# Optimization experiments

Measured on AMD Instinct MI355X. Metric: run time of the kernel, lower is better.

Reference implementation:

```python
import jax, jax.numpy as jnp
import numpy as np

N_EDGES = 262144
N_TRIP = 1048576
D = 128
N_RBF = 6
A_DIM = 49  # n_spher * l_spher
N_BIL = 8


def setup_inputs() -> dict:
    key = jax.random.key(0)
    ks = jax.random.split(key, 16)
    s = lambda fan_in: 1.0 / np.sqrt(fan_in)
    return {
        "m_ji": jax.random.normal(ks[0], (N_EDGES, D), jnp.float32),
        "e_rbf": jax.random.normal(ks[1], (N_EDGES, N_RBF), jnp.float32),
        "a_sbf": jax.random.normal(ks[2], (N_TRIP, A_DIM), jnp.float32),
        "nbr_list": jax.random.randint(ks[3], (N_EDGES, 2), 0, 100000),
        "angle_list": jax.random.randint(ks[4], (N_TRIP, 3), 0, N_EDGES),
        "kj_idx": jax.random.randint(ks[5], (N_TRIP,), 0, N_EDGES),
        "nbr_m_w": jax.random.normal(ks[6], (D, D), jnp.float32) * s(D),
        "nbr_m_b": jnp.zeros((D,), jnp.float32),
        "e_rbf_w": jax.random.normal(ks[7], (N_RBF, D), jnp.float32) * s(N_RBF),
        "a_sbf_w": jax.random.normal(ks[8], (A_DIM, N_BIL), jnp.float32) * s(A_DIM),
        "final_w": jax.random.normal(ks[9], (D, N_BIL, D), jnp.float32) * s(N_BIL * D),
        "m_ji_w": jax.random.normal(ks[10], (D, D), jnp.float32) * s(D),
        "m_ji_b": jnp.zeros((D,), jnp.float32),
        "post_w": jax.random.normal(ks[11], (D, D), jnp.float32) * s(D),
        "post_b": jnp.zeros((D,), jnp.float32),
        "res_w": jax.random.normal(ks[12], (3, 2, D, D), jnp.float32) * s(D),
        "res_b": jnp.zeros((3, 2, D), jnp.float32),
    }


def _residual(x, w2, b2):
    # two Dense(swish) layers + skip
    out = x
    for k in range(2):
        out = jax.nn.silu(out @ w2[k] + b2[k])
    return out + x


def reference(m_ji, e_rbf, a_sbf, nbr_list, angle_list, kj_idx,
              nbr_m_w, nbr_m_b, e_rbf_w, a_sbf_w, final_w,
              m_ji_w, m_ji_b, post_w, post_b, res_w, res_b):
    # DirectedMessage: gather per-triplet edge features
    t_m = jax.nn.silu(m_ji[kj_idx] @ nbr_m_w + nbr_m_b)   # [W, D]
    t_e = e_rbf[kj_idx] @ e_rbf_w                          # [W, D]
    m_and_e = t_m * t_e                                    # [W, D]
    t_a = a_sbf @ a_sbf_w                                  # [W, J]
    out = jnp.einsum('wj,wl,ijl->wi', t_a, m_and_e, final_w)  # [W, D]
    directed = jax.ops.segment_sum(out, kj_idx, num_segments=m_ji.shape[0])  # [E, D]

    transf_m_ji = jax.nn.silu(m_ji @ m_ji_w + m_ji_b)
    output = directed + transf_m_ji
    output = _residual(output, res_w[0], res_b[0])
    output = jax.nn.silu(output @ post_w + post_b) + transf_m_ji
    output = _residual(output, res_w[1], res_b[1])
    output = _residual(output, res_w[2], res_b[2])
    return output
```

## Files before the change

kernel.cpp:

```cpp
#include <hip/hip_runtime.h>

#define N_EDGE 262144
#define N_TRI  1048576
#define DIM    128
#define NRBF   6
#define ADIM   49
#define NBIL   8
#define TE     64
#define TP     2
#define NTHR   256
#define SXD    68
#define EB2    2048
#define NSL    4

typedef __attribute__((ext_vector_type(8))) short bf16x8;
typedef __attribute__((ext_vector_type(4))) float f32x4;

__device__ __forceinline__ float fast_rcp(float x) {
    float r; asm("v_rcp_f32 %0, %1" : "=v"(r) : "v"(x)); return r;
}
__device__ __forceinline__ float fast_exp2(float x) {
    float r; asm("v_exp_f32 %0, %1" : "=v"(r) : "v"(x)); return r;
}
__device__ __forceinline__ float silu_f(float x) {
    return x * fast_rcp(1.f + fast_exp2(-1.44269504f * x));
}
__device__ __forceinline__ unsigned short f2bf(float f) {
    unsigned int u = __float_as_uint(f);
    return (unsigned short)((u + 0x7FFFu + ((u >> 16) & 1u)) >> 16);
}
__device__ __forceinline__ unsigned int pk2(float x, float y) {
    unsigned int r;
    asm("v_cvt_pk_bf16_f32 %0, %1, %2" : "=v"(r) : "v"(x), "v"(y));
    return r;
}
__device__ __forceinline__ float bf2f(unsigned short u) {
    return __uint_as_float(((unsigned int)u) << 16);
}

__global__ __launch_bounds__(256) void prep_w_k(
    const float* __restrict__ nbr, const float* __restrict__ mji,
    const float* __restrict__ post, const float* __restrict__ res,
    const float* __restrict__ fw, unsigned short* __restrict__ wt)
{
    int idx = blockIdx.x * 256 + threadIdx.x;
    if (idx < 9 * 16384) {
        int m = idx >> 14, rr = idx & 16383;
        int n = rr >> 7, ks = rr & 127;
        int ko = (ks & ~31) | ((ks & 1) << 4) | ((ks >> 1) & 15);
        const float* src = (m == 0) ? nbr : (m == 1) ? mji : (m == 2) ? post
                          : (res + (size_t)(m - 3) * 16384);
        wt[idx] = f2bf(src[ko * DIM + n]);
    } else {
        int r2 = idx - 9 * 16384;
        int n = r2 >> 10, j = (r2 >> 7) & 7, ls = r2 & 127;
        int lo = (ls & ~31) | ((ls & 1) << 4) | ((ls >> 1) & 15);
        wt[idx] = f2bf(fw[(size_t)(n * NBIL + j) * DIM + lo]);
    }
}

__global__ __launch_bounds__(256) void ta_all_k(
    const float* __restrict__ a_sbf, const float* __restrict__ a_sbf_w,
    float* __restrict__ taw)
{
    __shared__ __align__(16) float sA[256 * ADIM];
    __shared__ float sWa[ADIM * NBIL];
    const int tid = threadIdx.x;
    const size_t w0 = (size_t)blockIdx.x * 256;

    {
        const float4* src = (const float4*)(a_sbf + w0 * ADIM);
        float4* dst = (float4*)sA;
        for (int i = tid; i < (256 * ADIM) / 4; i += 256) dst[i] = src[i];
    }
    for (int i = tid; i < ADIM * NBIL; i += 256) sWa[i] = a_sbf_w[i];
    __syncthreads();

    float ta[NBIL];
    #pragma unroll
    for (int j = 0; j < NBIL; ++j) ta[j] = 0.0f;
    const float* row = sA + tid * ADIM;
    #pragma unroll
    for (int k = 0; k < ADIM; ++k) {
        float v = row[k];
        #pragma unroll
        for (int j = 0; j < NBIL; ++j) ta[j] = fmaf(v, sWa[k * NBIL + j], ta[j]);
    }
    float4* dst = (float4*)(taw + (w0 + tid) * NBIL);
    dst[0] = make_float4(ta[0], ta[1], ta[2], ta[3]);
    dst[1] = make_float4(ta[4], ta[5], ta[6], ta[7]);
}

__global__ __launch_bounds__(1024) void seg_reduce_k(
    const float* __restrict__ taw, const int* __restrict__ kj_idx,
    float* __restrict__ ta_sum)
{
    __shared__ float acc[EB2 * NBIL];
    const int tid = threadIdx.x;
    const int eg = blockIdx.x >> 2;
    const int sl = blockIdx.x & 3;
    const int lo = eg * EB2;

    for (int i = tid; i < EB2 * NBIL; i += 1024) acc[i] = 0.f;
    __syncthreads();

    const int4* kj4 = (const int4*)kj_idx;
    const int i0 = sl * (N_TRI / 4 / NSL);
    const int i1 = i0 + (N_TRI / 4 / NSL);
    for (int i = i0 + tid; i < i1; i += 1024) {
        int4 v = kj4[i];
        int w0 = i * 4;
        #pragma unroll
        for (int k = 0; k < 4; ++k) {
            int e = (k == 0) ? v.x : (k == 1) ? v.y : (k == 2) ? v.z : v.w;
            unsigned d = (unsigned)(e - lo);
            if (d < (unsigned)EB2) {
                const float4* p = (const float4*)(taw + (size_t)(w0 + k) * NBIL);
                float4 a = p[0], b = p[1];
                float* q = acc + d * NBIL;
                atomicAdd(q + 0, a.x); atomicAdd(q + 1, a.y);
                atomicAdd(q + 2, a.z); atomicAdd(q + 3, a.w);
                atomicAdd(q + 4, b.x); atomicAdd(q + 5, b.y);
                atomicAdd(q + 6, b.z); atomicAdd(q + 7, b.w);
            }
        }
    }
    __syncthreads();
    for (int i = tid; i < EB2 * NBIL; i += 1024)
        unsafeAtomicAdd(ta_sum + (size_t)lo * NBIL + i, acc[i]);
}

__global__ __launch_bounds__(256) void triplet_atomic_k(
    const float* __restrict__ a_sbf, const float* __restrict__ a_sbf_w,
    const int* __restrict__ kj_idx, float* __restrict__ ta_sum)
{
    __shared__ __align__(16) float sA[256 * ADIM];
    __shared__ float sWa[ADIM * NBIL];
    const int tid = threadIdx.x;
    const size_t w0 = (size_t)blockIdx.x * 256;
    {
        const float4* src = (const float4*)(a_sbf + w0 * ADIM);
        float4* dst = (float4*)sA;
        for (int i = tid; i < (256 * ADIM) / 4; i += 256) dst[i] = src[i];
    }
    for (int i = tid; i < ADIM * NBIL; i += 256) sWa[i] = a_sbf_w[i];
    __syncthreads();
    float ta[NBIL];
    #pragma unroll
    for (int j = 0; j < NBIL; ++j) ta[j] = 0.0f;
    const float* row = sA + tid * ADIM;
    #pragma unroll
    for (int k = 0; k < ADIM; ++k) {
        float v = row[k];
        #pragma unroll
        for (int j = 0; j < NBIL; ++j) ta[j] = fmaf(v, sWa[k * NBIL + j], ta[j]);
    }
    const int e = kj_idx[w0 + tid];
    float* dst = ta_sum + (size_t)e * NBIL;
    #pragma unroll
    for (int j = 0; j < NBIL; ++j) unsafeAtomicAdd(dst + j, ta[j]);
}

__global__ __launch_bounds__(NTHR) void edge_main_k(
    const float* __restrict__ m_ji, const float* __restrict__ e_rbf,
    const float* __restrict__ ta_sum, const unsigned short* __restrict__ wt,
    const float* __restrict__ nbr_m_b, const float* __restrict__ e_rbf_w,
    const float* __restrict__ m_ji_b, const float* __restrict__ post_b,
    const float* __restrict__ res_b, float* __restrict__ out)
{
    __shared__ __align__(16) unsigned int sXdA[TP * TE * SXD];
    __shared__ __align__(16) unsigned int sTdA[TP * TE * SXD];
    __shared__ __align__(16) float sTAT[NBIL * TP * TE];
    __shared__ __align__(16) float sET[NRBF * TP * TE];

    const int tid  = threadIdx.x;
    const int lane = tid & 63;
    const int ml   = lane & 15;
    const int g    = lane >> 4;
    const int wq   = tid >> 6;
    const int n0   = wq * 32;
    const int q16  = wq * 16;
    const size_t e0 = (size_t)blockIdx.x * (TP * TE);
    const int ET = TP * TE;

    bf16x8 A[4][2], Bf[2][4];
    f32x4 acc0[4][2], acc1[4][2], xr0[4][2], xr1[4][2], bs0, bs1;

    auto prefB = [&](const unsigned short* wtm, int ldk, int kbase) {
        #pragma unroll
        for (int nt = 0; nt < 2; ++nt) {
            const unsigned short* wb =
                wtm + (size_t)(n0 + nt * 16 + ml) * ldk + kbase + g * 8;
            #pragma unroll
            for (int ks = 0; ks < 4; ++ks)
                Bf[nt][ks] = *(const bf16x8*)(wb + ks * 32);
        }
    };
    auto ldbias = [&](const float* bp) {
        float b0 = bp[n0 + ml], b1 = bp[n0 + 16 + ml];
        bs0[0] = b0; bs0[1] = b0; bs0[2] = b0; bs0[3] = b0;
        bs1[0] = b1; bs1[1] = b1; bs1[2] = b1; bs1[3] = b1;
    };
    auto ldzero = [&]() {
        #pragma unroll
        for (int r = 0; r < 4; ++r) { bs0[r] = 0.f; bs1[r] = 0.f; }
    };

    prefB(wt + 1 * 16384, DIM, 0);

    #pragma unroll
    for (int i = 0; i < 8; ++i) {
        int q = tid + i * NTHR;
        int row = q >> 4, sub = q & 15;
        int dq = sub >> 2, c4 = (sub & 3) * 4;
        const float* src = m_ji + (e0 + row) * DIM + dq * 32 + c4;
        float4 a = *(const float4*)(src);
        float4 b = *(const float4*)(src + 16);
        uint4 d;
        d.x = pk2(a.x, b.x); d.y = pk2(a.y, b.y);
        d.z = pk2(a.z, b.z); d.w = pk2(a.w, b.w);
        *(uint4*)(sXdA + row * SXD + dq * 16 + c4) = d;
    }
    #pragma unroll
    for (int i = 0; i < 4; ++i) {
        int idx = tid + i * NTHR;
        int j = idx >> 7, e = idx & 127;
        sTAT[j * ET + e] = ta_sum[(e0 + e) * NBIL + j];
    }
    for (int i = tid; i < NRBF * ET; i += NTHR) {
        int j = i >> 7, e = i & 127;
        sET[j * ET + e] = e_rbf[(e0 + e) * NRBF + j];
    }
    __syncthreads();

    auto loadA = [&](const unsigned int* bufp, int h) {
        const unsigned short* base = (const unsigned short*)bufp;
        #pragma unroll
        for (int mt = 0; mt < 4; ++mt) {
            const unsigned short* rb = base + (mt * 16 + ml) * (SXD * 2) + h * 64 + g * 8;
            A[mt][0] = *(const bf16x8*)(rb);
            A[mt][1] = *(const bf16x8*)(rb + 32);
        }
    };
    auto mfmaH = [&](f32x4 (&acc)[4][2], int h, bool seed) {
        #pragma unroll
        for (int kk = 0; kk < 2; ++kk)
        #pragma unroll
        for (int nt = 0; nt < 2; ++nt)
        #pragma unroll
        for (int mt = 0; mt < 4; ++mt) {
            f32x4 cin = (seed && kk == 0) ? (nt == 0 ? bs0 : bs1) : acc[mt][nt];
            acc[mt][nt] = __builtin_amdgcn_mfma_f32_16x16x32_bf16(
                A[mt][kk], Bf[nt][h * 2 + kk], cin, 0, 0, 0);
        }
    };
    auto gemm_full = [&](const unsigned int* bufp, f32x4 (&acc)[4][2]) {
        loadA(bufp, 0); mfmaH(acc, 0, true); loadA(bufp, 1); mfmaH(acc, 1, false);
    };
    auto store_pair = [&](f32x4 (&v0)[4][2], f32x4 (&v1)[4][2]) {
        __syncthreads();
        #pragma unroll
        for (int mt = 0; mt < 4; ++mt)
        #pragma unroll
        for (int r = 0; r < 4; ++r) {
            int off = (mt * 16 + g * 4 + r) * SXD + q16 + ml;
            sXdA[off]               = pk2(v0[mt][0][r], v0[mt][1][r]);
            sXdA[TE * SXD + off]    = pk2(v1[mt][0][r], v1[mt][1][r]);
        }
        __syncthreads();
    };

    const unsigned int* b0p = sXdA;
    const unsigned int* b1p = sXdA + TE * SXD;

    ldbias(m_ji_b);
    gemm_full(b0p, acc0);
    gemm_full(b1p, acc1);
    prefB(wt + 0 * 16384, DIM, 0);
    #pragma unroll
    for (int mt = 0; mt < 4; ++mt)
    #pragma unroll
    for (int r = 0; r < 4; ++r) {
        int off = (mt * 16 + g * 4 + r) * SXD + q16 + ml;
        sTdA[off]            = pk2(silu_f(acc0[mt][0][r]), silu_f(acc0[mt][1][r]));
        sTdA[TE * SXD + off] = pk2(silu_f(acc1[mt][0][r]), silu_f(acc1[mt][1][r]));
    }

    ldbias(nbr_m_b);
    float ewc[2][NRBF];
    #pragma unroll
    for (int nt = 0; nt < 2; ++nt)
    #pragma unroll
    for (int q = 0; q < NRBF; ++q)
        ewc[nt][q] = e_rbf_w[q * DIM + n0 + nt * 16 + ml];
    gemm_full(b0p, acc0);
    gemm_full(b1p, acc1);
    const unsigned short* fwb = wt + 9 * 16384;
    prefB(fwb, NBIL * DIM, 0);
    #pragma unroll
    for (int t = 0; t < 2; ++t) {
        f32x4 (&ac)[4][2] = (t == 0) ? acc0 : acc1;
        #pragma unroll
        for (int mt = 0; mt < 4; ++mt) {
            f32x4 er[NRBF];
            #pragma unroll
            for (int q = 0; q < NRBF; ++q)
                er[q] = *(const f32x4*)(sET + q * ET + t * TE + mt * 16 + g * 4);
            #pragma unroll
            for (int r = 0; r < 4; ++r) {
                float te0 = 0.f, te1 = 0.f;
                #pragma unroll
                for (int q = 0; q < NRBF; ++q) {
                    te0 = fmaf(er[q][r], ewc[0][q], te0);
                    te1 = fmaf(er[q][r], ewc[1][q], te1);
                }
                ac[mt][0][r] = silu_f(ac[mt][0][r]) * te0;
                ac[mt][1][r] = silu_f(ac[mt][1][r]) * te1;
            }
        }
    }
    store_pair(acc0, acc1);

    #pragma unroll
    for (int mt = 0; mt < 4; ++mt)
    #pragma unroll
    for (int r = 0; r < 4; ++r) {
        int off = (mt * 16 + g * 4 + r) * SXD + q16 + ml;
        unsigned int t0 = sTdA[off], t1 = sTdA[TE * SXD + off];
        xr0[mt][0][r] = bf2f((unsigned short)(t0 & 0xffff));
        xr0[mt][1][r] = bf2f((unsigned short)(t0 >> 16));
        xr1[mt][0][r] = bf2f((unsigned short)(t1 & 0xffff));
        xr1[mt][1][r] = bf2f((unsigned short)(t1 >> 16));
    }
    ldzero();
    for (int j = 0; j < NBIL; ++j) {
        gemm_full(b0p, acc0);
        gemm_full(b1p, acc1);
        if (j < NBIL - 1) prefB(fwb, NBIL * DIM, (j + 1) * DIM);
        else              prefB(wt + 3 * 16384, DIM, 0);
        #pragma unroll
        for (int mt = 0; mt < 4; ++mt) {
            f32x4 tv0 = *(const f32x4*)(sTAT + j * ET + mt * 16 + g * 4);
            f32x4 tv1 = *(const f32x4*)(sTAT + j * ET + TE + mt * 16 + g * 4);
            #pragma unroll
            for (int nt = 0; nt < 2; ++nt)
            #pragma unroll
            for (int r = 0; r < 4; ++r) {
                xr0[mt][nt][r] = fmaf(tv0[r], acc0[mt][nt][r], xr0[mt][nt][r]);
                xr1[mt][nt][r] = fmaf(tv1[r], acc1[mt][nt][r], xr1[mt][nt][r]);
            }
        }
    }
    store_pair(xr0, xr1);

    auto silu_inplace = [&](f32x4 (&ac)[4][2]) {
        #pragma unroll
        for (int mt = 0; mt < 4; ++mt)
        #pragma unroll
        for (int r = 0; r < 4; ++r) {
            ac[mt][0][r] = silu_f(ac[mt][0][r]);
            ac[mt][1][r] = silu_f(ac[mt][1][r]);
        }
    };
    auto add_into = [&](f32x4 (&xr)[4][2], f32x4 (&ac)[4][2]) {
        #pragma unroll
        for (int mt = 0; mt < 4; ++mt)
        #pragma unroll
        for (int r = 0; r < 4; ++r) {
            xr[mt][0][r] += silu_f(ac[mt][0][r]);
            xr[mt][1][r] += silu_f(ac[mt][1][r]);
        }
    };

    ldbias(res_b + 0);
    gemm_full(b0p, acc0); gemm_full(b1p, acc1); prefB(wt + 4 * 16384, DIM, 0);
    silu_inplace(acc0); silu_inplace(acc1);
    store_pair(acc0, acc1);
    ldbias(res_b + 128);
    gemm_full(b0p, acc0); gemm_full(b1p, acc1); prefB(wt + 2 * 16384, DIM, 0);
    add_into(xr0, acc0); add_into(xr1, acc1);
    store_pair(xr0, xr1);

    ldbias(post_b);
    gemm_full(b0p, acc0); gemm_full(b1p, acc1); prefB(wt + 5 * 16384, DIM, 0);
    #pragma unroll
    for (int mt = 0; mt < 4; ++mt)
    #pragma unroll
    for (int r = 0; r < 4; ++r) {
        int off = (mt * 16 + g * 4 + r) * SXD + q16 + ml;
        unsigned int t0 = sTdA[off], t1 = sTdA[TE * SXD + off];
        xr0[mt][0][r] = silu_f(acc0[mt][0][r]) + bf2f((unsigned short)(t0 & 0xffff));
        xr0[mt][1][r] = silu_f(acc0[mt][1][r]) + bf2f((unsigned short)(t0 >> 16));
        xr1[mt][0][r] = silu_f(acc1[mt][0][r]) + bf2f((unsigned short)(t1 & 0xffff));
        xr1[mt][1][r] = silu_f(acc1[mt][1][r]) + bf2f((unsigned short)(t1 >> 16));
    }
    store_pair(xr0, xr1);

    ldbias(res_b + 256);
    gemm_full(b0p, acc0); gemm_full(b1p, acc1); prefB(wt + 6 * 16384, DIM, 0);
    silu_inplace(acc0); silu_inplace(acc1);
    store_pair(acc0, acc1);
    ldbias(res_b + 384);
    gemm_full(b0p, acc0); gemm_full(b1p, acc1); prefB(wt + 7 * 16384, DIM, 0);
    add_into(xr0, acc0); add_into(xr1, acc1);
    store_pair(xr0, xr1);

    ldbias(res_b + 512);
    gemm_full(b0p, acc0); gemm_full(b1p, acc1); prefB(wt + 8 * 16384, DIM, 0);
    silu_inplace(acc0); silu_inplace(acc1);
    store_pair(acc0, acc1);
    ldbias(res_b + 640);
    gemm_full(b0p, acc0); gemm_full(b1p, acc1);
    #pragma unroll
    for (int mt = 0; mt < 4; ++mt)
    #pragma unroll
    for (int r = 0; r < 4; ++r) {
        int row = mt * 16 + g * 4 + r;
        out[(e0 + row) * DIM + n0 + ml]           = silu_f(acc0[mt][0][r]) + xr0[mt][0][r];
        out[(e0 + row) * DIM + n0 + 16 + ml]      = silu_f(acc0[mt][1][r]) + xr0[mt][1][r];
        out[(e0 + TE + row) * DIM + n0 + ml]      = silu_f(acc1[mt][0][r]) + xr1[mt][0][r];
        out[(e0 + TE + row) * DIM + n0 + 16 + ml] = silu_f(acc1[mt][1][r]) + xr1[mt][1][r];
    }
}

extern "C" void kernel_launch(void* const* d_in, const int* in_sizes, int n_in,
                              void* d_out, int out_size, void* d_ws, size_t ws_size,
                              hipStream_t stream)
{
    (void)in_sizes; (void)n_in; (void)out_size;
    const float* m_ji    = (const float*)d_in[0];
    const float* e_rbf   = (const float*)d_in[1];
    const float* a_sbf   = (const float*)d_in[2];
    const int*   kj_idx  = (const int*)d_in[5];
    const float* nbr_m_w = (const float*)d_in[6];
    const float* nbr_m_b = (const float*)d_in[7];
    const float* e_rbf_w = (const float*)d_in[8];
    const float* a_sbf_w = (const float*)d_in[9];
    const float* final_w = (const float*)d_in[10];
    const float* m_ji_w  = (const float*)d_in[11];
    const float* m_ji_b  = (const float*)d_in[12];
    const float* post_w  = (const float*)d_in[13];
    const float* post_b  = (const float*)d_in[14];
    const float* res_w   = (const float*)d_in[15];
    const float* res_b   = (const float*)d_in[16];
    float* out = (float*)d_out;

    const size_t taB  = (size_t)N_EDGE * NBIL * sizeof(float);
    const size_t wtB  = (size_t)278528 * sizeof(unsigned short);
    const size_t tawB = (size_t)N_TRI * NBIL * sizeof(float);

    float* ta_sum = (float*)d_ws;
    unsigned short* wt = (unsigned short*)((char*)d_ws + taB);
    float* taw = (float*)((char*)d_ws + taB + wtB);

    prep_w_k<<<1088, 256, 0, stream>>>(nbr_m_w, m_ji_w, post_w, res_w, final_w, wt);
    hipMemsetAsync(ta_sum, 0, taB, stream);

    if (ws_size >= taB + wtB + tawB) {
        ta_all_k<<<N_TRI / 256, 256, 0, stream>>>(a_sbf, a_sbf_w, taw);
        seg_reduce_k<<<(N_EDGE / EB2) * NSL, 1024, 0, stream>>>(taw, kj_idx, ta_sum);
    } else {
        triplet_atomic_k<<<N_TRI / 256, 256, 0, stream>>>(a_sbf, a_sbf_w, kj_idx, ta_sum);
    }
    edge_main_k<<<N_EDGE / (TP * TE), NTHR, 0, stream>>>(m_ji, e_rbf, ta_sum, wt,
        nbr_m_b, e_rbf_w, m_ji_b, post_b, res_b, out);
}
```

Baseline: 489.0 us.

## Keep residuals in shared bf16 ping-pong buffers to cut register pressure

The fp32 residual accumulators xr0/xr1 no longer live in registers across the post-MLP chain. The residual is kept as bf16 in shared memory and updated in place through two alternating buffers, which also removes one barrier per layer. The transformed m_ji is packed into registers instead of a dedicated shared array. The bilinear loop now runs per 64-row tile, so the final_w fragments are reloaded twice. The intent is lower VGPR use and fewer syncs, at the cost of extra weight loads and residuals rounded to bf16 between layers.

```diff
diff --git a/kernel.cpp b/kernel.cpp
--- a/kernel.cpp
+++ b/kernel.cpp
@@ -8,6 +8,7 @@
 #define NBIL   8
 #define TE     64
 #define TP     2
+#define ET     (TP * TE)
 #define NTHR   256
 #define SXD    68
 #define EB2    2048
@@ -168,10 +169,10 @@
     const float* __restrict__ m_ji_b, const float* __restrict__ post_b,
     const float* __restrict__ res_b, float* __restrict__ out)
 {
-    __shared__ __align__(16) unsigned int sXdA[TP * TE * SXD];
-    __shared__ __align__(16) unsigned int sTdA[TP * TE * SXD];
-    __shared__ __align__(16) float sTAT[NBIL * TP * TE];
-    __shared__ __align__(16) float sET[NRBF * TP * TE];
+    __shared__ __align__(16) unsigned int b0[ET * SXD];
+    __shared__ __align__(16) unsigned int b1[ET * SXD];
+    __shared__ __align__(16) float sTAT[NBIL * ET];
+    __shared__ __align__(16) float sET[NRBF * ET];
 
     const int tid  = threadIdx.x;
     const int lane = tid & 63;
@@ -180,11 +181,11 @@
     const int wq   = tid >> 6;
     const int n0   = wq * 32;
     const int q16  = wq * 16;
-    const size_t e0 = (size_t)blockIdx.x * (TP * TE);
-    const int ET = TP * TE;
+    const size_t e0 = (size_t)blockIdx.x * ET;
 
     bf16x8 A[4][2], Bf[2][4];
-    f32x4 acc0[4][2], acc1[4][2], xr0[4][2], xr1[4][2], bs0, bs1;
+    f32x4 acc0[4][2], acc1[4][2], bs0, bs1;
+    unsigned int trp0[4][4], trp1[4][4];
 
     auto prefB = [&](const unsigned short* wtm, int ldk, int kbase) {
         #pragma unroll
@@ -197,9 +198,9 @@
         }
     };
     auto ldbias = [&](const float* bp) {
-        float b0 = bp[n0 + ml], b1 = bp[n0 + 16 + ml];
-        bs0[0] = b0; bs0[1] = b0; bs0[2] = b0; bs0[3] = b0;
-        bs1[0] = b1; bs1[1] = b1; bs1[2] = b1; bs1[3] = b1;
+        float v0 = bp[n0 + ml], v1 = bp[n0 + 16 + ml];
+        bs0[0] = v0; bs0[1] = v0; bs0[2] = v0; bs0[3] = v0;
+        bs1[0] = v1; bs1[1] = v1; bs1[2] = v1; bs1[3] = v1;
     };
     auto ldzero = [&]() {
         #pragma unroll
@@ -219,7 +220,7 @@
         uint4 d;
         d.x = pk2(a.x, b.x); d.y = pk2(a.y, b.y);
         d.z = pk2(a.z, b.z); d.w = pk2(a.w, b.w);
-        *(uint4*)(sXdA + row * SXD + dq * 16 + c4) = d;
+        *(uint4*)(b0 + row * SXD + dq * 16 + c4) = d;
     }
     #pragma unroll
     for (int i = 0; i < 4; ++i) {
@@ -233,11 +234,12 @@
     }
     __syncthreads();
 
-    auto loadA = [&](const unsigned int* bufp, int h) {
+    auto loadA = [&](const unsigned int* bufp, int t, int h) {
         const unsigned short* base = (const unsigned short*)bufp;
         #pragma unroll
         for (int mt = 0; mt < 4; ++mt) {
-            const unsigned short* rb = base + (mt * 16 + ml) * (SXD * 2) + h * 64 + g * 8;
+            const unsigned short* rb =
+                base + (t * 64 + mt * 16 + ml) * (SXD * 2) + h * 64 + g * 8;
             A[mt][0] = *(const bf16x8*)(rb);
             A[mt][1] = *(const bf16x8*)(rb + 32);
         }
@@ -254,172 +256,194 @@
                 A[mt][kk], Bf[nt][h * 2 + kk], cin, 0, 0, 0);
         }
     };
-    auto gemm_full = [&](const unsigned int* bufp, f32x4 (&acc)[4][2]) {
-        loadA(bufp, 0); mfmaH(acc, 0, true); loadA(bufp, 1); mfmaH(acc, 1, false);
-    };
-    auto store_pair = [&](f32x4 (&v0)[4][2], f32x4 (&v1)[4][2]) {
-        __syncthreads();
+    auto gemm_full = [&](const unsigned int* bufp, int t, f32x4 (&acc)[4][2]) {
+        loadA(bufp, t, 0); mfmaH(acc, 0, true);
+        loadA(bufp, t, 1); mfmaH(acc, 1, false);
+    };
+    auto store_tile = [&](unsigned int* bufp, int t, f32x4 (&v)[4][2]) {
         #pragma unroll
         for (int mt = 0; mt < 4; ++mt)
         #pragma unroll
-        for (int r = 0; r < 4; ++r) {
-            int off = (mt * 16 + g * 4 + r) * SXD + q16 + ml;
-            sXdA[off]               = pk2(v0[mt][0][r], v0[mt][1][r]);
-            sXdA[TE * SXD + off]    = pk2(v1[mt][0][r], v1[mt][1][r]);
-        }
-        __syncthreads();
-    };
-
-    const unsigned int* b0p = sXdA;
-    const unsigned int* b1p = sXdA + TE * SXD;
+        for (int r = 0; r < 4; ++r)
+            bufp[(t * 64 + mt * 16 + g * 4 + r) * SXD + q16 + ml] =
+                pk2(v[mt][0][r], v[mt][1][r]);
+    };
 
     ldbias(m_ji_b);
-    gemm_full(b0p, acc0);
-    gemm_full(b1p, acc1);
+    gemm_full(b0, 0, acc0);
+    gemm_full(b0, 1, acc1);
     prefB(wt + 0 * 16384, DIM, 0);
     #pragma unroll
     for (int mt = 0; mt < 4; ++mt)
     #pragma unroll
     for (int r = 0; r < 4; ++r) {
-        int off = (mt * 16 + g * 4 + r) * SXD + q16 + ml;
-        sTdA[off]            = pk2(silu_f(acc0[mt][0][r]), silu_f(acc0[mt][1][r]));
-        sTdA[TE * SXD + off] = pk2(silu_f(acc1[mt][0][r]), silu_f(acc1[mt][1][r]));
+        trp0[mt][r] = pk2(silu_f(acc0[mt][0][r]), silu_f(acc0[mt][1][r]));
+        trp1[mt][r] = pk2(silu_f(acc1[mt][0][r]), silu_f(acc1[mt][1][r]));
     }
 
     ldbias(nbr_m_b);
-    float ewc[2][NRBF];
-    #pragma unroll
-    for (int nt = 0; nt < 2; ++nt)
-    #pragma unroll
-    for (int q = 0; q < NRBF; ++q)
-        ewc[nt][q] = e_rbf_w[q * DIM + n0 + nt * 16 + ml];
-    gemm_full(b0p, acc0);
-    gemm_full(b1p, acc1);
+    gemm_full(b0, 0, acc0);
+    gemm_full(b0, 1, acc1);
     const unsigned short* fwb = wt + 9 * 16384;
     prefB(fwb, NBIL * DIM, 0);
+    {
+        float ewc[2][NRBF];
+        #pragma unroll
+        for (int nt = 0; nt < 2; ++nt)
+        #pragma unroll
+        for (int q = 0; q < NRBF; ++q)
+            ewc[nt][q] = e_rbf_w[q * DIM + n0 + nt * 16 + ml];
+        #pragma unroll
+        for (int t = 0; t < 2; ++t) {
+            f32x4 (&ac)[4][2] = (t == 0) ? acc0 : acc1;
+            #pragma unroll
+            for (int mt = 0; mt < 4; ++mt) {
+                f32x4 er[NRBF];
+                #pragma unroll
+                for (int q = 0; q < NRBF; ++q)
+                    er[q] = *(const f32x4*)(sET + q * ET + t * 64 + mt * 16 + g * 4);
+                #pragma unroll
+                for (int r = 0; r < 4; ++r) {
+                    float te0 = 0.f, te1 = 0.f;
+                    #pragma unroll
+                    for (int q = 0; q < NRBF; ++q) {
+                        te0 = fmaf(er[q][r], ewc[0][q], te0);
+                        te1 = fmaf(er[q][r], ewc[1][q], te1);
+                    }
+                    ac[mt][0][r] = silu_f(ac[mt][0][r]) * te0;
+                    ac[mt][1][r] = silu_f(ac[mt][1][r]) * te1;
+                }
+            }
+        }
+    }
+    store_tile(b1, 0, acc0);
+    store_tile(b1, 1, acc1);
+    __syncthreads();
+
+    ldzero();
     #pragma unroll
     for (int t = 0; t < 2; ++t) {
+        f32x4 xr[4][2];
+        #pragma unroll
+        for (int mt = 0; mt < 4; ++mt)
+        #pragma unroll
+        for (int r = 0; r < 4; ++r) {
+            unsigned int tv = (t == 0) ? trp0[mt][r] : trp1[mt][r];
+            xr[mt][0][r] = bf2f((unsigned short)(tv & 0xffff));
+            xr[mt][1][r] = bf2f((unsigned short)(tv >> 16));
+        }
+        for (int j = 0; j < NBIL; ++j) {
+            gemm_full(b1, t, acc0);
+            if (j < NBIL - 1)      prefB(fwb, NBIL * DIM, (j + 1) * DIM);
+            else if (t == 0)       prefB(fwb, NBIL * DIM, 0);
+            else                   prefB(wt + 3 * 16384, DIM, 0);
+            #pragma unroll
+            for (int mt = 0; mt < 4; ++mt) {
+                f32x4 tv = *(const f32x4*)(sTAT + j * ET + t * 64 + mt * 16 + g * 4);
+                #pragma unroll
+                for (int nt = 0; nt < 2; ++nt)
+                #pragma unroll
+                for (int r = 0; r < 4; ++r)
+                    xr[mt][nt][r] = fmaf(tv[r], acc0[mt][nt][r], xr[mt][nt][r]);
+            }
+        }
+        store_tile(b0, t, xr);
+    }
+    __syncthreads();
+
+    auto silu_both = [&]() {
+        #pragma unroll
+        for (int mt = 0; mt < 4; ++mt)
+        #pragma unroll
+        for (int r = 0; r < 4; ++r) {
+            acc0[mt][0][r] = silu_f(acc0[mt][0][r]);
+            acc0[mt][1][r] = silu_f(acc0[mt][1][r]);
+            acc1[mt][0][r] = silu_f(acc1[mt][0][r]);
+            acc1[mt][1][r] = silu_f(acc1[mt][1][r]);
+        }
+    };
+    auto xupdate = [&](unsigned int* xbuf) {
+        #pragma unroll
+        for (int t = 0; t < 2; ++t)
+        #pragma unroll
+        for (int mt = 0; mt < 4; ++mt)
+        #pragma unroll
+        for (int r = 0; r < 4; ++r) {
+            int off = (t * 64 + mt * 16 + g * 4 + r) * SXD + q16 + ml;
+            unsigned int xo = xbuf[off];
+            f32x4 (&ac)[4][2] = (t == 0) ? acc0 : acc1;
+            float v0 = bf2f((unsigned short)(xo & 0xffff)) + silu_f(ac[mt][0][r]);
+            float v1 = bf2f((unsigned short)(xo >> 16))    + silu_f(ac[mt][1][r]);
+            xbuf[off] = pk2(v0, v1);
+        }
+        __syncthreads();
+    };
+
+    ldbias(res_b + 0);
+    gemm_full(b0, 0, acc0); gemm_full(b0, 1, acc1);
+    prefB(wt + 4 * 16384, DIM, 0);
+    silu_both();
+    store_tile(b1, 0, acc0); store_tile(b1, 1, acc1);
+    __syncthreads();
+
+    ldbias(res_b + 128);
+    gemm_full(b1, 0, acc0); gemm_full(b1, 1, acc1);
+    prefB(wt + 2 * 16384, DIM, 0);
+    xupdate(b0);
+
+    ldbias(post_b);
+    gemm_full(b0, 0, acc0); gemm_full(b0, 1, acc1);
+    prefB(wt + 5 * 16384, DIM, 0);
+    #pragma unroll
+    for (int t = 0; t < 2; ++t)
+    #pragma unroll
+    for (int mt = 0; mt < 4; ++mt)
+    #pragma unroll
+    for (int r = 0; r < 4; ++r) {
+        int off = (t * 64 + mt * 16 + g * 4 + r) * SXD + q16 + ml;
+        unsigned int tv = (t == 0) ? trp0[mt][r] : trp1[mt][r];
         f32x4 (&ac)[4][2] = (t == 0) ? acc0 : acc1;
-        #pragma unroll
-        for (int mt = 0; mt < 4; ++mt) {
-            f32x4 er[NRBF];
-            #pragma unroll
-            for (int q = 0; q < NRBF; ++q)
-                er[q] = *(const f32x4*)(sET + q * ET + t * TE + mt * 16 + g * 4);
-            #pragma unroll
-            for (int r = 0; r < 4; ++r) {
-                float te0 = 0.f, te1 = 0.f;
-                #pragma unroll
-                for (int q = 0; q < NRBF; ++q) {
-                    te0 = fmaf(er[q][r], ewc[0][q], te0);
-                    te1 = fmaf(er[q][r], ewc[1][q], te1);
-                }
-                ac[mt][0][r] = silu_f(ac[mt][0][r]) * te0;
-                ac[mt][1][r] = silu_f(ac[mt][1][r]) * te1;
-            }
-        }
-    }
-    store_pair(acc0, acc1);
-
+        float v0 = silu_f(ac[mt][0][r]) + bf2f((unsigned short)(tv & 0xffff));
+        float v1 = silu_f(ac[mt][1][r]) + bf2f((unsigned short)(tv >> 16));
+        b1[off] = pk2(v0, v1);
+    }
+    __syncthreads();
+
+    ldbias(res_b + 256);
+    gemm_full(b1, 0, acc0); gemm_full(b1, 1, acc1);
+    prefB(wt + 6 * 16384, DIM, 0);
+    silu_both();
+    store_tile(b0, 0, acc0); store_tile(b0, 1, acc1);
+    __syncthreads();
+
+    ldbias(res_b + 384);
+    gemm_full(b0, 0, acc0); gemm_full(b0, 1, acc1);
+    prefB(wt + 7 * 16384, DIM, 0);
+    xupdate(b1);
+
+    ldbias(res_b + 512);
+    gemm_full(b1, 0, acc0); gemm_full(b1, 1, acc1);
+    prefB(wt + 8 * 16384, DIM, 0);
+    silu_both();
+    store_tile(b0, 0, acc0); store_tile(b0, 1, acc1);
+    __syncthreads();
+
+    ldbias(res_b + 640);
+    gemm_full(b0, 0, acc0); gemm_full(b0, 1, acc1);
+    #pragma unroll
+    for (int t = 0; t < 2; ++t)
     #pragma unroll
     for (int mt = 0; mt < 4; ++mt)
     #pragma unroll
     for (int r = 0; r < 4; ++r) {
-        int off = (mt * 16 + g * 4 + r) * SXD + q16 + ml;
-        unsigned int t0 = sTdA[off], t1 = sTdA[TE * SXD + off];
-        xr0[mt][0][r] = bf2f((unsigned short)(t0 & 0xffff));
-        xr0[mt][1][r] = bf2f((unsigned short)(t0 >> 16));
-        xr1[mt][0][r] = bf2f((unsigned short)(t1 & 0xffff));
-        xr1[mt][1][r] = bf2f((unsigned short)(t1 >> 16));
-    }
-    ldzero();
-    for (int j = 0; j < NBIL; ++j) {
-        gemm_full(b0p, acc0);
-        gemm_full(b1p, acc1);
-        if (j < NBIL - 1) prefB(fwb, NBIL * DIM, (j + 1) * DIM);
-        else              prefB(wt + 3 * 16384, DIM, 0);
-        #pragma unroll
-        for (int mt = 0; mt < 4; ++mt) {
-            f32x4 tv0 = *(const f32x4*)(sTAT + j * ET + mt * 16 + g * 4);
-            f32x4 tv1 = *(const f32x4*)(sTAT + j * ET + TE + mt * 16 + g * 4);
-            #pragma unroll
-            for (int nt = 0; nt < 2; ++nt)
-            #pragma unroll
-            for (int r = 0; r < 4; ++r) {
-                xr0[mt][nt][r] = fmaf(tv0[r], acc0[mt][nt][r], xr0[mt][nt][r]);
-                xr1[mt][nt][r] = fmaf(tv1[r], acc1[mt][nt][r], xr1[mt][nt][r]);
-            }
-        }
-    }
-    store_pair(xr0, xr1);
-
-    auto silu_inplace = [&](f32x4 (&ac)[4][2]) {
-        #pragma unroll
-        for (int mt = 0; mt < 4; ++mt)
-        #pragma unroll
-        for (int r = 0; r < 4; ++r) {
-            ac[mt][0][r] = silu_f(ac[mt][0][r]);
-            ac[mt][1][r] = silu_f(ac[mt][1][r]);
-        }
-    };
-    auto add_into = [&](f32x4 (&xr)[4][2], f32x4 (&ac)[4][2]) {
-        #pragma unroll
-        for (int mt = 0; mt < 4; ++mt)
-        #pragma unroll
-        for (int r = 0; r < 4; ++r) {
-            xr[mt][0][r] += silu_f(ac[mt][0][r]);
-            xr[mt][1][r] += silu_f(ac[mt][1][r]);
-        }
-    };
-
-    ldbias(res_b + 0);
-    gemm_full(b0p, acc0); gemm_full(b1p, acc1); prefB(wt + 4 * 16384, DIM, 0);
-    silu_inplace(acc0); silu_inplace(acc1);
-    store_pair(acc0, acc1);
-    ldbias(res_b + 128);
-    gemm_full(b0p, acc0); gemm_full(b1p, acc1); prefB(wt + 2 * 16384, DIM, 0);
-    add_into(xr0, acc0); add_into(xr1, acc1);
-    store_pair(xr0, xr1);
-
-    ldbias(post_b);
-    gemm_full(b0p, acc0); gemm_full(b1p, acc1); prefB(wt + 5 * 16384, DIM, 0);
-    #pragma unroll
-    for (int mt = 0; mt < 4; ++mt)
-    #pragma unroll
-    for (int r = 0; r < 4; ++r) {
-        int off = (mt * 16 + g * 4 + r) * SXD + q16 + ml;
-        unsigned int t0 = sTdA[off], t1 = sTdA[TE * SXD + off];
-        xr0[mt][0][r] = silu_f(acc0[mt][0][r]) + bf2f((unsigned short)(t0 & 0xffff));
-        xr0[mt][1][r] = silu_f(acc0[mt][1][r]) + bf2f((unsigned short)(t0 >> 16));
-        xr1[mt][0][r] = silu_f(acc1[mt][0][r]) + bf2f((unsigned short)(t1 & 0xffff));
-        xr1[mt][1][r] = silu_f(acc1[mt][1][r]) + bf2f((unsigned short)(t1 >> 16));
-    }
-    store_pair(xr0, xr1);
-
-    ldbias(res_b + 256);
-    gemm_full(b0p, acc0); gemm_full(b1p, acc1); prefB(wt + 6 * 16384, DIM, 0);
-    silu_inplace(acc0); silu_inplace(acc1);
-    store_pair(acc0, acc1);
-    ldbias(res_b + 384);
-    gemm_full(b0p, acc0); gemm_full(b1p, acc1); prefB(wt + 7 * 16384, DIM, 0);
-    add_into(xr0, acc0); add_into(xr1, acc1);
-    store_pair(xr0, xr1);
-
-    ldbias(res_b + 512);
-    gemm_full(b0p, acc0); gemm_full(b1p, acc1); prefB(wt + 8 * 16384, DIM, 0);
-    silu_inplace(acc0); silu_inplace(acc1);
-    store_pair(acc0, acc1);
-    ldbias(res_b + 640);
-    gemm_full(b0p, acc0); gemm_full(b1p, acc1);
-    #pragma unroll
-    for (int mt = 0; mt < 4; ++mt)
-    #pragma unroll
-    for (int r = 0; r < 4; ++r) {
-        int row = mt * 16 + g * 4 + r;
-        out[(e0 + row) * DIM + n0 + ml]           = silu_f(acc0[mt][0][r]) + xr0[mt][0][r];
-        out[(e0 + row) * DIM + n0 + 16 + ml]      = silu_f(acc0[mt][1][r]) + xr0[mt][1][r];
-        out[(e0 + TE + row) * DIM + n0 + ml]      = silu_f(acc1[mt][0][r]) + xr1[mt][0][r];
-        out[(e0 + TE + row) * DIM + n0 + 16 + ml] = silu_f(acc1[mt][1][r]) + xr1[mt][1][r];
+        int row = t * 64 + mt * 16 + g * 4 + r;
+        int off = row * SXD + q16 + ml;
+        unsigned int xo = b1[off];
+        f32x4 (&ac)[4][2] = (t == 0) ? acc0 : acc1;
+        out[(e0 + row) * DIM + n0 + ml] =
+            silu_f(ac[mt][0][r]) + bf2f((unsigned short)(xo & 0xffff));
+        out[(e0 + row) * DIM + n0 + 16 + ml] =
+            silu_f(ac[mt][1][r]) + bf2f((unsigned short)(xo >> 16));
     }
 }
 
@@ -462,6 +486,6 @@
     } else {
         triplet_atomic_k<<<N_TRI / 256, 256, 0, stream>>>(a_sbf, a_sbf_w, kj_idx, ta_sum);
     }
-    edge_main_k<<<N_EDGE / (TP * TE), NTHR, 0, stream>>>(m_ji, e_rbf, ta_sum, wt,
+    edge_main_k<<<N_EDGE / ET, NTHR, 0, stream>>>(m_ji, e_rbf, ta_sum, wt,
         nbr_m_b, e_rbf_w, m_ji_b, post_b, res_b, out);
 }
```

After: 524.3 us. 7.2% more time.
